# Kernel optimization log

Measured on AMD Instinct MI355X. Metric: run time of the kernel, lower is better.

The kernel has to match this reference:

```python
import jax
import jax.numpy as jnp
import numpy as np
from functools import partial

B, C_CLS, H, W = 1, 2, 480, 854
KS = (7, 7, 9)       # kernel sizes of the 3 pairwise kernels
DILS = (64, 16, 1)   # their dilations
STEPS = 5            # PacCRFLoose: independent params per mean-field step


def unfold2d(x, k, dil):
    """x: [B,C,H,W] -> [B,C,k*k,H,W]: zero-padded dilated k x k neighborhoods."""
    b, c, h, w = x.shape
    pad = (k // 2) * dil
    xp = jnp.pad(x, ((0, 0), (0, 0), (pad, pad), (pad, pad)))
    taps = [xp[:, :, i * dil:i * dil + h, j * dil:j * dil + w]
            for i in range(k) for j in range(k)]
    return jnp.stack(taps, axis=2)


@partial(jax.checkpoint, static_argnums=(1, 2))
def pac_kernel(feat, k, dil):
    """Fixed Gaussian pixel-adaptive kernel exp(-0.5*||f_p - f_q||^2): [B,k*k,H,W]."""
    d = unfold2d(feat, k, dil) - feat[:, :, None]  # center tap diff is 0 -> kernel 1
    return jnp.exp(-0.5 * jnp.sum(d * d, axis=1))


def message(Q, K, k, dil, filt):
    """PacConv2d with shared spatial filter: sum_t w_t * K_t(p) * Q(p + off_t)."""
    Qc = unfold2d(Q, k, dil)  # [B, C, T, H, W]
    return jnp.einsum('bcthw,bthw,t->bchw', Qc, K, filt)


def crf_forward(unary, x, feat_scales, potts_w, unary_weights, pw_weights,
                w_filt0, w_filt1, w_filt2, compat0, compat1):
    b, _, h, w = x.shape
    yy, xx = jnp.meshgrid(jnp.arange(h, dtype=x.dtype),
                          jnp.arange(w, dtype=x.dtype), indexing='ij')
    mesh = jnp.broadcast_to(jnp.stack([yy, xx])[None], (b, 2, h, w))

    # create_YXRGB: channels [y/s0, x/s1, r/s2, g/s3, b/s4]
    feats = [jnp.concatenate([mesh / feat_scales[i, :2, None, None],
                              x / feat_scales[i, 2:, None, None]], axis=1)
             for i in range(3)]
    # create_position_feats appended as 4th edge feature; PacCRF only consumes
    # edge_feat[0..n_kernels-1] so it is dead in the original forward too.
    _pos = mesh * (1.0 / potts_w.reshape(-1, 1, 1))

    # edge kernels are computed once (PacCRFLoose shares them across steps)
    kernels = [pac_kernel(feats[i], KS[i], DILS[i]) for i in range(3)]

    unary5 = unary * 5.0  # ModelWithCrf scales unary by 5 before the CRF

    def step(logQ, p):
        uw, pw, w0, w1, w2, c0, c1 = p
        Q = jax.nn.softmax(logQ, axis=1)
        m0 = jnp.einsum('dc,bchw->bdhw', c0, message(Q, kernels[0], KS[0], DILS[0], w0))
        m1 = jnp.einsum('dc,bchw->bdhw', c1, message(Q, kernels[1], KS[1], DILS[1], w1))
        m2 = message(Q, kernels[2], KS[2], DILS[2], w2)  # potts: no compat conv
        new_logQ = uw * unary5 + pw[0] * m0 + pw[1] * m1 + pw[2] * m2
        return new_logQ, None

    logQ, _ = jax.lax.scan(jax.checkpoint(step), unary5,
                           (unary_weights, pw_weights, w_filt0, w_filt1, w_filt2,
                            compat0, compat1))
    return logQ  # final_output='log_Q'


def setup_inputs():
    key = jax.random.key(0)
    k = jax.random.split(key, 8)
    unary = jax.random.normal(k[0], (B, C_CLS, H, W), jnp.float32)
    x = jax.random.uniform(k[1], (B, 3, H, W), jnp.float32) * 255.0  # RGB frame
    # p_sc = ((5-1)*16+1)/4 = 16.25, c_sc = 30.0 for all 3 scale sets (as in source)
    feat_scales = jnp.tile(jnp.array([16.25, 16.25, 30.0, 30.0, 30.0],
                                     jnp.float32)[None], (3, 1))
    potts_w = jnp.ones((1,), jnp.float32)
    unary_weights = jnp.full((STEPS,), 0.85, jnp.float32)
    pw_weights = jnp.tile(jnp.array([1.0, 1.0, 6.0], jnp.float32)[None], (STEPS, 1))
    pr = 0.001  # perturbed_init range
    w_filt0 = 1.0 / 49 + (jax.random.uniform(k[2], (STEPS, 49)) - 0.5) * pr
    w_filt1 = 1.0 / 49 + (jax.random.uniform(k[3], (STEPS, 49)) - 0.5) * pr
    w_filt2 = 1.0 / 81 + (jax.random.uniform(k[4], (STEPS, 81)) - 0.5) * pr
    off_diag = (1.0 - jnp.eye(C_CLS, dtype=jnp.float32))[None]
    compat0 = off_diag + (jax.random.uniform(k[5], (STEPS, C_CLS, C_CLS)) - 0.5) * pr
    compat1 = off_diag + (jax.random.uniform(k[6], (STEPS, C_CLS, C_CLS)) - 0.5) * pr
    return dict(unary=unary, x=x, feat_scales=feat_scales, potts_w=potts_w,
                unary_weights=unary_weights, pw_weights=pw_weights,
                w_filt0=w_filt0, w_filt1=w_filt1, w_filt2=w_filt2,
                compat0=compat0, compat1=compat1)


def reference(unary, x, feat_scales, potts_w, unary_weights, pw_weights,
              w_filt0, w_filt1, w_filt2, compat0, compat1):
    return crf_forward(unary, x, feat_scales, potts_w, unary_weights, pw_weights,
                       w_filt0, w_filt1, w_filt2, compat0, compat1)
```

## Files before the change

kernel.cpp:

```cpp
#include <hip/hip_runtime.h>

typedef _Float16 h2 __attribute__((ext_vector_type(2)));

#define HH 480
#define WW 854
#define HWSZ (HH * WW)
#define PAD 192
#define PSTR 1240
#define PH (HH + 2 * PAD)
#define PCELLS (PH * PSTR)
#define TPSTRIDE 240

#if __has_builtin(__builtin_amdgcn_exp2f)
#define EXP2(x) __builtin_amdgcn_exp2f(x)
#else
#define EXP2(x) exp2f(x)
#endif

__device__ __forceinline__ float fdot2f(h2 a, h2 b, float c)
{
#if __has_builtin(__builtin_amdgcn_fdot2)
    return __builtin_amdgcn_fdot2(a, b, c, false);
#else
    return fmaf((float)a.x, (float)b.x, fmaf((float)a.y, (float)b.y, c));
#endif
}

__device__ __forceinline__ h2 bch2(unsigned u)
{
    union { unsigned u; h2 h; } v; v.u = u; return v.h;
}
__device__ __forceinline__ unsigned h2u(h2 h)
{
    union { h2 h; unsigned u; } v; v.h = h; return v.u;
}
__device__ __forceinline__ float hiq(unsigned u)
{
    union { unsigned u; h2 h; } v; v.u = u; return (float)v.h.y;
}
__device__ __forceinline__ unsigned short hbits(_Float16 h)
{
    union { _Float16 h; unsigned short u; } v; v.h = h; return v.u;
}

__global__ __launch_bounds__(256) void init_P(
    const float* __restrict__ xrgb, const float* __restrict__ fs,
    uint2* __restrict__ PA, uint2* __restrict__ PB)
{
    int i = blockIdx.x * 256 + threadIdx.x;
    if (i >= PCELLS) return;
    int y = i / PSTR, x = i - y * PSTR;
    int iy = y - PAD, ix = x - PAD;
    uint2 v;
    if (iy >= 0 && iy < HH && ix >= 0 && ix < WW) {
        int p = iy * WW + ix;
        _Float16 rh = (_Float16)(xrgb[p] * (1.0f / fs[2]));
        _Float16 gh = (_Float16)(xrgb[HWSZ + p] * (1.0f / fs[3]));
        _Float16 bh = (_Float16)(xrgb[2 * HWSZ + p] * (1.0f / fs[4]));
        v = make_uint2(h2u(h2{rh, gh}), h2u(h2{bh, (_Float16)0}));
    } else {
        v = make_uint2(0x7BFF7BFFu, 0x00007BFFu);
    }
    PA[i] = v;
    PB[i] = v;
}

__global__ __launch_bounds__(256) void pack0(
    const float* __restrict__ unary, unsigned* __restrict__ PAw)
{
    int i = blockIdx.x * 256 + threadIdx.x;
    if (i >= HWSZ) return;
    float l0 = unary[i], l1 = unary[HWSZ + i];
    float q = 1.0f / (1.0f + __expf(5.0f * (l1 - l0)));
    int y = i / WW, x = i - y * WW;
    int c = (y + PAD) * PSTR + x + PAD;
    unsigned old = PAw[2 * c + 1];
    PAw[2 * c + 1] = (old & 0xFFFFu) | ((unsigned)hbits((_Float16)q) << 16);
}

__global__ __launch_bounds__(256) void build_tp(
    const float* __restrict__ fs, const float* __restrict__ uwArr,
    const float* __restrict__ pwArr,
    const float* __restrict__ w0, const float* __restrict__ w1,
    const float* __restrict__ w2,
    const float* __restrict__ c0, const float* __restrict__ c1,
    float* __restrict__ tp)
{
    int s = blockIdx.x;
    int t = threadIdx.x;
    float* d = tp + s * TPSTRIDE;
    const float NH = -0.72134752044448169f;

    if (t < 49) {
        int dy = t / 7 - 3, dx = t % 7 - 3;
        float py = dy * 64.0f / fs[0], px = dx * 64.0f / fs[1];
        d[(t / 7) * 8 + t % 7] =
            log2f(w0[s * 49 + t]) + NH * (py * py + px * px);
    } else if (t >= 64 && t < 113) {
        int u = t - 64;
        int dy = u / 7 - 3, dx = u % 7 - 3;
        float py = dy * 16.0f / fs[5], px = dx * 16.0f / fs[6];
        d[56 + (u / 7) * 8 + u % 7] =
            log2f(w1[s * 49 + u]) + NH * (py * py + px * px);
    } else if (t >= 128 && t < 209) {
        int u = t - 128;
        int dy = u / 9 - 4, dx = u % 9 - 4;
        float py = dy / fs[10], px = dx / fs[11];
        d[112 + (u / 9) * 12 + u % 9] =
            log2f(w2[s * 81 + u]) + NH * (py * py + px * px);
    } else if (t == 224) {
        float r1 = fs[2] / fs[7], r2 = fs[2] / fs[12];
        d[220] = NH;
        d[221] = NH * r1 * r1;
        d[222] = NH * r2 * r2;
        d[223] = c0[s * 4 + 0];  d[224] = c0[s * 4 + 1];
        d[225] = c0[s * 4 + 2];  d[226] = c0[s * 4 + 3];
        d[227] = c1[s * 4 + 0];  d[228] = c1[s * 4 + 1];
        d[229] = c1[s * 4 + 2];  d[230] = c1[s * 4 + 3];
        d[231] = pwArr[s * 3 + 0];
        d[232] = pwArr[s * 3 + 1];
        d[233] = pwArr[s * 3 + 2];
        d[234] = uwArr[s] * 5.0f;
    }
}

__device__ __forceinline__ void tap8(uint2 aq, h2 rgp, h2 bqp, float nk,
                                     float tpv, float& A, float& B)
{
    h2 drg = bch2(aq.x) - rgp;
    h2 dbq = bch2(aq.y) - bqp;
    h2 dbm = bch2(h2u(dbq) & 0xFFFFu);
    float s1 = fdot2f(drg, drg, 0.0f);
    float ssq = fdot2f(dbm, dbm, s1);
    float e = EXP2(fmaf(ssq, nk, tpv));
    A = fmaf(e, hiq(aq.y), A);
    B += e;
}

template <int T0, int N>
__device__ __forceinline__ void loadK0(uint2 (&buf)[N], const uint2* __restrict__ Pc)
{
#pragma unroll
    for (int t = 0; t < N; ++t) {
        const int tt = T0 + t;
        buf[t] = Pc[(tt / 7 - 3) * 64 * PSTR + (tt % 7 - 3) * 64];
    }
}
template <int T0, int N>
__device__ __forceinline__ void compK0(const uint2 (&buf)[N],
                                       const float* __restrict__ tp0,
                                       h2 rgp, h2 bqp, float nk,
                                       float& A, float& B)
{
#pragma unroll
    for (int t = 0; t < N; ++t) {
        const int tt = T0 + t;
        tap8(buf[t], rgp, bqp, nk, tp0[(tt / 7) * 8 + tt % 7], A, B);
    }
}
template <int T0, int N>
__device__ __forceinline__ void compK2(const uint2* __restrict__ T2b,
                                       const float* __restrict__ tp2,
                                       h2 rgp, h2 bqp, float nk,
                                       float& A, float& B)
{
#pragma unroll
    for (int t = 0; t < N; ++t) {
        const int tt = T0 + t;
        tap8(T2b[(tt / 9) * 136 + tt % 9], rgp, bqp, nk,
             tp2[(tt / 9) * 12 + tt % 9], A, B);
    }
}

template <bool LAST>
__global__ __launch_bounds__(256, 3) void crf_step(
    const uint2* __restrict__ srcP, unsigned* __restrict__ dstPw,
    const float* __restrict__ unary, const float* __restrict__ tpAll,
    int step, float* __restrict__ out)
{
    __shared__ uint2 T1[14 * 224];
    __shared__ uint2 T2[10 * 136];

    int tid = threadIdx.y * 128 + threadIdx.x;
    int x0 = blockIdx.x * 128, y0 = blockIdx.y * 2;

#pragma unroll
    for (int r = 0; r < 14; ++r) {
        if (tid < 112) {
            int gy = y0 + 16 * (r >> 1) + (r & 1) - 48;
            const uint4* srow = (const uint4*)
                (srcP + (gy + PAD) * PSTR + (x0 - 48 + PAD));
            ((uint4*)T1)[r * 112 + tid] = srow[tid];
        }
    }
#pragma unroll
    for (int r = 0; r < 10; ++r) {
        int t2 = tid - 128;
        if (t2 >= 0 && t2 < 68) {
            int gy = y0 - 4 + r;
            const uint4* srow = (const uint4*)
                (srcP + (gy + PAD) * PSTR + (x0 - 4 + PAD));
            ((uint4*)T2)[r * 68 + t2] = srow[t2];
        }
    }
    __syncthreads();

    int x = x0 + threadIdx.x;
    int y = y0 + threadIdx.y;
    if (x >= WW) return;
    int p = y * WW + x;
    int ccell = (y + PAD) * PSTR + x + PAD;

    const float* tp0 = tpAll + step * TPSTRIDE;
    const float* tp1 = tp0 + 56;
    const float* tp2 = tp0 + 112;
    const float* sc  = tp0 + 220;
    float nk0 = sc[0], nk1 = sc[1], nk2 = sc[2];

    float un0 = unary[p], un1 = unary[HWSZ + p];

    const uint2* Pc = srcP + ccell;
    uint2 cw = *Pc;
    h2 rgp = bch2(cw.x);
    h2 bqp = bch2(cw.y);

    const uint2* T1b = T1 + threadIdx.y * 224 + threadIdx.x;
    const uint2* T2b = T2 + threadIdx.y * 136 + threadIdx.x;

    float A0 = 0.f, B0 = 0.f, A1 = 0.f, B1 = 0.f, A2 = 0.f, B2 = 0.f;

    uint2 bA[13], bB[12], bC[12], bD[12];
    loadK0<0, 13>(bA, Pc);
    compK2<0, 20>(T2b, tp2, rgp, bqp, nk2, A2, B2);
    loadK0<13, 12>(bB, Pc);
    compK0<0, 13>(bA, tp0, rgp, bqp, nk0, A0, B0);
    compK2<20, 20>(T2b, tp2, rgp, bqp, nk2, A2, B2);
    loadK0<25, 12>(bC, Pc);
    compK0<13, 12>(bB, tp0, rgp, bqp, nk0, A0, B0);
    compK2<40, 20>(T2b, tp2, rgp, bqp, nk2, A2, B2);
    loadK0<37, 12>(bD, Pc);
    compK0<25, 12>(bC, tp0, rgp, bqp, nk0, A0, B0);
    compK2<60, 21>(T2b, tp2, rgp, bqp, nk2, A2, B2);
    compK0<37, 12>(bD, tp0, rgp, bqp, nk0, A0, B0);

#pragma unroll
    for (int i = 0; i < 7; ++i)
#pragma unroll
        for (int j = 0; j < 7; ++j)
            tap8(T1b[i * 448 + j * 16], rgp, bqp, nk1,
                 tp1[i * 8 + j], A1, B1);

    float m00 = A0, m01 = B0 - A0;
    float m10 = A1, m11 = B1 - A1;
    float m20 = A2, m21 = B2 - A2;

    float r00 = sc[3] * m00 + sc[4] * m01;
    float r01 = sc[5] * m00 + sc[6] * m01;
    float r10 = sc[7] * m10 + sc[8] * m11;
    float r11 = sc[9] * m10 + sc[10] * m11;

    float pw0 = sc[11], pw1 = sc[12], pw2 = sc[13], uw5 = sc[14];
    float o0 = uw5 * un0 + pw0 * r00 + pw1 * r10 + pw2 * m20;
    float o1 = uw5 * un1 + pw0 * r01 + pw1 * r11 + pw2 * m21;

    if (LAST) {
        out[p] = o0;
        out[HWSZ + p] = o1;
    } else {
        float qn = 1.0f / (1.0f + __expf(o1 - o0));
        unsigned nb = (h2u(bqp) & 0xFFFFu) |
                      ((unsigned)hbits((_Float16)qn) << 16);
        dstPw[2 * ccell + 1] = nb;
    }
}

extern "C" void kernel_launch(void* const* d_in, const int* in_sizes, int n_in,
                              void* d_out, int out_size, void* d_ws, size_t ws_size,
                              hipStream_t stream)
{
    const float* unary = (const float*)d_in[0];
    const float* xrgb  = (const float*)d_in[1];
    const float* fs    = (const float*)d_in[2];
    const float* uw    = (const float*)d_in[4];
    const float* pw    = (const float*)d_in[5];
    const float* w0    = (const float*)d_in[6];
    const float* w1    = (const float*)d_in[7];
    const float* w2    = (const float*)d_in[8];
    const float* c0    = (const float*)d_in[9];
    const float* c1    = (const float*)d_in[10];
    float* out = (float*)d_out;

    uint2* PA = (uint2*)d_ws;
    uint2* PB = (uint2*)((char*)d_ws + (size_t)PCELLS * 8);
    float* tpAll = (float*)((char*)d_ws + (size_t)PCELLS * 16);

    init_P<<<(PCELLS + 255) / 256, 256, 0, stream>>>(xrgb, fs, PA, PB);
    pack0<<<(HWSZ + 255) / 256, 256, 0, stream>>>(unary, (unsigned*)PA);
    build_tp<<<5, 256, 0, stream>>>(fs, uw, pw, w0, w1, w2, c0, c1, tpAll);

    dim3 gs((WW + 127) / 128, HH / 2), bs(128, 2);
    for (int s = 0; s < 5; ++s) {
        const uint2* src = (s & 1) ? PB : PA;
        unsigned* dst = (unsigned*)((s & 1) ? PA : PB);
        if (s < 4)
            crf_step<false><<<gs, bs, 0, stream>>>(src, dst, unary, tpAll,
                                                   s, out);
        else
            crf_step<true><<<gs, bs, 0, stream>>>(src, dst, unary, tpAll,
                                                  s, out);
    }
}
```

Before: 185.0 us.

## Issue dilated-tap global loads before barrier and interleave K1 taps

```diff
diff --git a/kernel.cpp b/kernel.cpp
--- a/kernel.cpp
+++ b/kernel.cpp
@@ -33,10 +33,6 @@
 __device__ __forceinline__ unsigned h2u(h2 h)
 {
     union { h2 h; unsigned u; } v; v.h = h; return v.u;
-}
-__device__ __forceinline__ float hiq(unsigned u)
-{
-    union { unsigned u; h2 h; } v; v.u = u; return (float)v.h.y;
 }
 __device__ __forceinline__ unsigned short hbits(_Float16 h)
 {
@@ -129,11 +125,11 @@
 {
     h2 drg = bch2(aq.x) - rgp;
     h2 dbq = bch2(aq.y) - bqp;
-    h2 dbm = bch2(h2u(dbq) & 0xFFFFu);
     float s1 = fdot2f(drg, drg, 0.0f);
-    float ssq = fdot2f(dbm, dbm, s1);
+    float db = (float)dbq.x;
+    float ssq = fmaf(db, db, s1);
     float e = EXP2(fmaf(ssq, nk, tpv));
-    A = fmaf(e, hiq(aq.y), A);
+    A = fmaf(e, (float)bch2(aq.y).y, A);
     B += e;
 }
 
@@ -159,6 +155,19 @@
     }
 }
 template <int T0, int N>
+__device__ __forceinline__ void compK1(const uint2* __restrict__ T1b,
+                                       const float* __restrict__ tp1,
+                                       h2 rgp, h2 bqp, float nk,
+                                       float& A, float& B)
+{
+#pragma unroll
+    for (int t = 0; t < N; ++t) {
+        const int tt = T0 + t;
+        tap8(T1b[(tt / 7) * 448 + (tt % 7) * 16], rgp, bqp, nk,
+             tp1[(tt / 7) * 8 + tt % 7], A, B);
+    }
+}
+template <int T0, int N>
 __device__ __forceinline__ void compK2(const uint2* __restrict__ T2b,
                                        const float* __restrict__ tp2,
                                        h2 rgp, h2 bqp, float nk,
@@ -173,7 +182,7 @@
 }
 
 template <bool LAST>
-__global__ __launch_bounds__(256, 3) void crf_step(
+__global__ __launch_bounds__(256, 4) void crf_step(
     const uint2* __restrict__ srcP, unsigned* __restrict__ dstPw,
     const float* __restrict__ unary, const float* __restrict__ tpAll,
     int step, float* __restrict__ out)
@@ -203,11 +212,9 @@
             ((uint4*)T2)[r * 68 + t2] = srow[t2];
         }
     }
-    __syncthreads();
 
     int x = x0 + threadIdx.x;
     int y = y0 + threadIdx.y;
-    if (x >= WW) return;
     int p = y * WW + x;
     int ccell = (y + PAD) * PSTR + x + PAD;
 
@@ -217,10 +224,19 @@
     const float* sc  = tp0 + 220;
     float nk0 = sc[0], nk1 = sc[1], nk2 = sc[2];
 
-    float un0 = unary[p], un1 = unary[HWSZ + p];
-
     const uint2* Pc = srcP + ccell;
-    uint2 cw = *Pc;
+    uint2 cw = make_uint2(0u, 0u);
+    float un0 = 0.f, un1 = 0.f;
+    uint2 bA[13];
+    bool act = (x < WW);
+    if (act) {
+        cw = *Pc;
+        un0 = unary[p]; un1 = unary[HWSZ + p];
+        loadK0<0, 13>(bA, Pc);
+    }
+    __syncthreads();
+    if (!act) return;
+
     h2 rgp = bch2(cw.x);
     h2 bqp = bch2(cw.y);
 
@@ -229,26 +245,20 @@
 
     float A0 = 0.f, B0 = 0.f, A1 = 0.f, B1 = 0.f, A2 = 0.f, B2 = 0.f;
 
-    uint2 bA[13], bB[12], bC[12], bD[12];
-    loadK0<0, 13>(bA, Pc);
+    uint2 bB[12], bC[12], bD[12];
+    loadK0<13, 12>(bB, Pc);
     compK2<0, 20>(T2b, tp2, rgp, bqp, nk2, A2, B2);
-    loadK0<13, 12>(bB, Pc);
     compK0<0, 13>(bA, tp0, rgp, bqp, nk0, A0, B0);
+    loadK0<25, 12>(bC, Pc);
     compK2<20, 20>(T2b, tp2, rgp, bqp, nk2, A2, B2);
-    loadK0<25, 12>(bC, Pc);
     compK0<13, 12>(bB, tp0, rgp, bqp, nk0, A0, B0);
+    loadK0<37, 12>(bD, Pc);
+    compK1<0, 25>(T1b, tp1, rgp, bqp, nk1, A1, B1);
+    compK0<25, 12>(bC, tp0, rgp, bqp, nk0, A0, B0);
     compK2<40, 20>(T2b, tp2, rgp, bqp, nk2, A2, B2);
-    loadK0<37, 12>(bD, Pc);
-    compK0<25, 12>(bC, tp0, rgp, bqp, nk0, A0, B0);
+    compK0<37, 12>(bD, tp0, rgp, bqp, nk0, A0, B0);
+    compK1<25, 24>(T1b, tp1, rgp, bqp, nk1, A1, B1);
     compK2<60, 21>(T2b, tp2, rgp, bqp, nk2, A2, B2);
-    compK0<37, 12>(bD, tp0, rgp, bqp, nk0, A0, B0);
-
-#pragma unroll
-    for (int i = 0; i < 7; ++i)
-#pragma unroll
-        for (int j = 0; j < 7; ++j)
-            tap8(T1b[i * 448 + j * 16], rgp, bqp, nk1,
-                 tp1[i * 8 + j], A1, B1);
 
     float m00 = A0, m01 = B0 - A0;
     float m10 = A1, m11 = B1 - A1;
```

Result: faster. 167.8 us (-9.3%).

## Process two horizontal pixels per thread with 128-bit loads and 4-row tiles

Applied to the files above, without the earlier changes.

```diff
diff --git a/kernel.cpp b/kernel.cpp
--- a/kernel.cpp
+++ b/kernel.cpp
@@ -33,10 +33,6 @@
 __device__ __forceinline__ unsigned h2u(h2 h)
 {
     union { h2 h; unsigned u; } v; v.h = h; return v.u;
-}
-__device__ __forceinline__ float hiq(unsigned u)
-{
-    union { unsigned u; h2 h; } v; v.u = u; return (float)v.h.y;
 }
 __device__ __forceinline__ unsigned short hbits(_Float16 h)
 {
@@ -129,87 +125,105 @@
 {
     h2 drg = bch2(aq.x) - rgp;
     h2 dbq = bch2(aq.y) - bqp;
-    h2 dbm = bch2(h2u(dbq) & 0xFFFFu);
     float s1 = fdot2f(drg, drg, 0.0f);
-    float ssq = fdot2f(dbm, dbm, s1);
+    float db = (float)dbq.x;
+    float ssq = fmaf(db, db, s1);
     float e = EXP2(fmaf(ssq, nk, tpv));
-    A = fmaf(e, hiq(aq.y), A);
+    A = fmaf(e, (float)bch2(aq.y).y, A);
     B += e;
 }
 
-template <int T0, int N>
-__device__ __forceinline__ void loadK0(uint2 (&buf)[N], const uint2* __restrict__ Pc)
+__device__ __forceinline__ void tapPair(uint4 a, h2 rg0, h2 bq0, h2 rg1, h2 bq1,
+                                        float nk, float tpv,
+                                        float& Aa, float& Ba, float& Ab, float& Bb)
+{
+    tap8(make_uint2(a.x, a.y), rg0, bq0, nk, tpv, Aa, Ba);
+    tap8(make_uint2(a.z, a.w), rg1, bq1, nk, tpv, Ab, Bb);
+}
+
+template <int I>
+__device__ __forceinline__ void loadRow64(uint4 (&buf)[7], const uint2* __restrict__ Pc)
 {
 #pragma unroll
-    for (int t = 0; t < N; ++t) {
-        const int tt = T0 + t;
-        buf[t] = Pc[(tt / 7 - 3) * 64 * PSTR + (tt % 7 - 3) * 64];
-    }
-}
-template <int T0, int N>
-__device__ __forceinline__ void compK0(const uint2 (&buf)[N],
-                                       const float* __restrict__ tp0,
-                                       h2 rgp, h2 bqp, float nk,
-                                       float& A, float& B)
+    for (int j = 0; j < 7; ++j)
+        buf[j] = *(const uint4*)(Pc + (I - 3) * 64 * PSTR + (j - 3) * 64);
+}
+template <int I>
+__device__ __forceinline__ void compRow64(const uint4 (&buf)[7],
+    const float* __restrict__ tp0, h2 rg0, h2 bq0, h2 rg1, h2 bq1, float nk,
+    float& Aa, float& Ba, float& Ab, float& Bb)
 {
 #pragma unroll
-    for (int t = 0; t < N; ++t) {
-        const int tt = T0 + t;
-        tap8(buf[t], rgp, bqp, nk, tp0[(tt / 7) * 8 + tt % 7], A, B);
-    }
-}
-template <int T0, int N>
-__device__ __forceinline__ void compK2(const uint2* __restrict__ T2b,
-                                       const float* __restrict__ tp2,
-                                       h2 rgp, h2 bqp, float nk,
-                                       float& A, float& B)
+    for (int j = 0; j < 7; ++j)
+        tapPair(buf[j], rg0, bq0, rg1, bq1, nk, tp0[I * 8 + j], Aa, Ba, Ab, Bb);
+}
+
+template <int I>
+__device__ __forceinline__ void compK1row(const uint4* __restrict__ T1l,
+    const float* __restrict__ tp1, h2 rg0, h2 bq0, h2 rg1, h2 bq1, float nk,
+    float& Aa, float& Ba, float& Ab, float& Bb)
 {
 #pragma unroll
-    for (int t = 0; t < N; ++t) {
-        const int tt = T0 + t;
-        tap8(T2b[(tt / 9) * 136 + tt % 9], rgp, bqp, nk,
-             tp2[(tt / 9) * 12 + tt % 9], A, B);
+    for (int j = 0; j < 7; ++j) {
+        uint4 a = T1l[I * 448 + 8 * j];
+        tapPair(a, rg0, bq0, rg1, bq1, nk, tp1[I * 8 + j], Aa, Ba, Ab, Bb);
+    }
+}
+
+template <int I>
+__device__ __forceinline__ void compK2row(const uint4* __restrict__ T2r,
+    const uint2* __restrict__ T2r2,
+    const float* __restrict__ tp2, h2 rg0, h2 bq0, h2 rg1, h2 bq1, float nk,
+    float& Aa, float& Ba, float& Ab, float& Bb)
+{
+#pragma unroll
+    for (int j = 0; j < 9; ++j) {
+        float tpv = tp2[I * 12 + j];
+        if ((j & 1) == 0) {
+            uint4 a = T2r[I * 68 + j / 2];
+            tapPair(a, rg0, bq0, rg1, bq1, nk, tpv, Aa, Ba, Ab, Bb);
+        } else {
+            uint2 c0 = T2r2[I * 136 + j];
+            uint2 c1 = T2r2[I * 136 + j + 1];
+            tap8(c0, rg0, bq0, nk, tpv, Aa, Ba);
+            tap8(c1, rg1, bq1, nk, tpv, Ab, Bb);
+        }
     }
 }
 
 template <bool LAST>
-__global__ __launch_bounds__(256, 3) void crf_step(
+__global__ __launch_bounds__(256, 2) void crf_step(
     const uint2* __restrict__ srcP, unsigned* __restrict__ dstPw,
     const float* __restrict__ unary, const float* __restrict__ tpAll,
     int step, float* __restrict__ out)
 {
-    __shared__ uint2 T1[14 * 224];
-    __shared__ uint2 T2[10 * 136];
-
-    int tid = threadIdx.y * 128 + threadIdx.x;
-    int x0 = blockIdx.x * 128, y0 = blockIdx.y * 2;
-
-#pragma unroll
-    for (int r = 0; r < 14; ++r) {
-        if (tid < 112) {
-            int gy = y0 + 16 * (r >> 1) + (r & 1) - 48;
-            const uint4* srow = (const uint4*)
-                (srcP + (gy + PAD) * PSTR + (x0 - 48 + PAD));
-            ((uint4*)T1)[r * 112 + tid] = srow[tid];
-        }
-    }
-#pragma unroll
-    for (int r = 0; r < 10; ++r) {
-        int t2 = tid - 128;
-        if (t2 >= 0 && t2 < 68) {
-            int gy = y0 - 4 + r;
-            const uint4* srow = (const uint4*)
-                (srcP + (gy + PAD) * PSTR + (x0 - 4 + PAD));
-            ((uint4*)T2)[r * 68 + t2] = srow[t2];
-        }
-    }
-    __syncthreads();
-
-    int x = x0 + threadIdx.x;
-    int y = y0 + threadIdx.y;
-    if (x >= WW) return;
-    int p = y * WW + x;
-    int ccell = (y + PAD) * PSTR + x + PAD;
+    __shared__ uint4 T1[28 * 112];
+    __shared__ uint4 T2[12 * 68];
+
+    int tx = threadIdx.x, ty = threadIdx.y;
+    int tid = ty * 64 + tx;
+    int x0 = blockIdx.x * 128, y0 = blockIdx.y * 4;
+
+    for (int c = tid; c < 28 * 112; c += 256) {
+        int r = c / 112, col = c - r * 112;
+        int gy = y0 + (r & 3) + 16 * ((r >> 2) - 3);
+        T1[c] = *(const uint4*)
+            (srcP + (gy + PAD) * PSTR + (x0 - 48 + PAD) + 2 * col);
+    }
+    for (int c = tid; c < 12 * 68; c += 256) {
+        int r = c / 68, col = c - r * 68;
+        int gy = y0 - 4 + r;
+        T2[c] = *(const uint4*)
+            (srcP + (gy + PAD) * PSTR + (x0 - 4 + PAD) + 2 * col);
+    }
+
+    int px = x0 + 2 * tx;
+    int y = y0 + ty;
+    bool act = (px < WW);
+    int p = y * WW + px;
+    int pSafe = act ? p : 0;
+    int ccell = (y + PAD) * PSTR + px + PAD;
+    const uint2* Pc = srcP + ccell;
 
     const float* tp0 = tpAll + step * TPSTRIDE;
     const float* tp1 = tp0 + 56;
@@ -217,60 +231,87 @@
     const float* sc  = tp0 + 220;
     float nk0 = sc[0], nk1 = sc[1], nk2 = sc[2];
 
-    float un0 = unary[p], un1 = unary[HWSZ + p];
-
-    const uint2* Pc = srcP + ccell;
-    uint2 cw = *Pc;
-    h2 rgp = bch2(cw.x);
-    h2 bqp = bch2(cw.y);
-
-    const uint2* T1b = T1 + threadIdx.y * 224 + threadIdx.x;
-    const uint2* T2b = T2 + threadIdx.y * 136 + threadIdx.x;
-
-    float A0 = 0.f, B0 = 0.f, A1 = 0.f, B1 = 0.f, A2 = 0.f, B2 = 0.f;
-
-    uint2 bA[13], bB[12], bC[12], bD[12];
-    loadK0<0, 13>(bA, Pc);
-    compK2<0, 20>(T2b, tp2, rgp, bqp, nk2, A2, B2);
-    loadK0<13, 12>(bB, Pc);
-    compK0<0, 13>(bA, tp0, rgp, bqp, nk0, A0, B0);
-    compK2<20, 20>(T2b, tp2, rgp, bqp, nk2, A2, B2);
-    loadK0<25, 12>(bC, Pc);
-    compK0<13, 12>(bB, tp0, rgp, bqp, nk0, A0, B0);
-    compK2<40, 20>(T2b, tp2, rgp, bqp, nk2, A2, B2);
-    loadK0<37, 12>(bD, Pc);
-    compK0<25, 12>(bC, tp0, rgp, bqp, nk0, A0, B0);
-    compK2<60, 21>(T2b, tp2, rgp, bqp, nk2, A2, B2);
-    compK0<37, 12>(bD, tp0, rgp, bqp, nk0, A0, B0);
-
-#pragma unroll
-    for (int i = 0; i < 7; ++i)
-#pragma unroll
-        for (int j = 0; j < 7; ++j)
-            tap8(T1b[i * 448 + j * 16], rgp, bqp, nk1,
-                 tp1[i * 8 + j], A1, B1);
-
-    float m00 = A0, m01 = B0 - A0;
-    float m10 = A1, m11 = B1 - A1;
-    float m20 = A2, m21 = B2 - A2;
-
-    float r00 = sc[3] * m00 + sc[4] * m01;
-    float r01 = sc[5] * m00 + sc[6] * m01;
-    float r10 = sc[7] * m10 + sc[8] * m11;
-    float r11 = sc[9] * m10 + sc[10] * m11;
+    uint4 cw = *(const uint4*)Pc;
+    float2 unc0 = *(const float2*)(unary + pSafe);
+    float2 unc1 = *(const float2*)(unary + HWSZ + pSafe);
+    uint4 bufA[7], bufB[7];
+    loadRow64<0>(bufA, Pc);
+    loadRow64<1>(bufB, Pc);
+    __syncthreads();
+
+    h2 rg0 = bch2(cw.x), bq0 = bch2(cw.y);
+    h2 rg1 = bch2(cw.z), bq1 = bch2(cw.w);
+
+    const uint4* T1l  = T1 + ty * 112 + tx;
+    const uint4* T2r  = T2 + ty * 68 + tx;
+    const uint2* T2r2 = (const uint2*)T2 + ty * 136 + 2 * tx;
+
+    float A0a = 0, B0a = 0, A0b = 0, B0b = 0;
+    float A1a = 0, B1a = 0, A1b = 0, B1b = 0;
+    float A2a = 0, B2a = 0, A2b = 0, B2b = 0;
+
+#define K2(I) compK2row<I>(T2r, T2r2, tp2, rg0, bq0, rg1, bq1, nk2, A2a, B2a, A2b, B2b)
+#define K1(I) compK1row<I>(T1l, tp1, rg0, bq0, rg1, bq1, nk1, A1a, B1a, A1b, B1b)
+#define K0C(B_, I) compRow64<I>(B_, tp0, rg0, bq0, rg1, bq1, nk0, A0a, B0a, A0b, B0b)
+
+    K2(0);
+    K0C(bufA, 0);  loadRow64<2>(bufA, Pc);
+    K2(1);
+    K1(0);
+    K0C(bufB, 1);  loadRow64<3>(bufB, Pc);
+    K2(2);
+    K1(1);
+    K0C(bufA, 2);  loadRow64<4>(bufA, Pc);
+    K2(3);
+    K1(2);
+    K0C(bufB, 3);  loadRow64<5>(bufB, Pc);
+    K2(4);
+    K1(3);
+    K0C(bufA, 4);  loadRow64<6>(bufA, Pc);
+    K2(5);
+    K1(4);
+    K0C(bufB, 5);
+    K2(6);
+    K1(5);
+    K0C(bufA, 6);
+    K2(7);
+    K1(6);
+    K2(8);
+
+#undef K2
+#undef K1
+#undef K0C
+
+    if (!act) return;
 
     float pw0 = sc[11], pw1 = sc[12], pw2 = sc[13], uw5 = sc[14];
-    float o0 = uw5 * un0 + pw0 * r00 + pw1 * r10 + pw2 * m20;
-    float o1 = uw5 * un1 + pw0 * r01 + pw1 * r11 + pw2 * m21;
+
+    float m01a = B0a - A0a, m11a = B1a - A1a, m21a = B2a - A2a;
+    float r00a = sc[3] * A0a + sc[4] * m01a;
+    float r01a = sc[5] * A0a + sc[6] * m01a;
+    float r10a = sc[7] * A1a + sc[8] * m11a;
+    float r11a = sc[9] * A1a + sc[10] * m11a;
+    float o0a = uw5 * unc0.x + pw0 * r00a + pw1 * r10a + pw2 * A2a;
+    float o1a = uw5 * unc1.x + pw0 * r01a + pw1 * r11a + pw2 * m21a;
+
+    float m01b = B0b - A0b, m11b = B1b - A1b, m21b = B2b - A2b;
+    float r00b = sc[3] * A0b + sc[4] * m01b;
+    float r01b = sc[5] * A0b + sc[6] * m01b;
+    float r10b = sc[7] * A1b + sc[8] * m11b;
+    float r11b = sc[9] * A1b + sc[10] * m11b;
+    float o0b = uw5 * unc0.y + pw0 * r00b + pw1 * r10b + pw2 * A2b;
+    float o1b = uw5 * unc1.y + pw0 * r01b + pw1 * r11b + pw2 * m21b;
 
     if (LAST) {
-        out[p] = o0;
-        out[HWSZ + p] = o1;
+        *(float2*)(out + p) = make_float2(o0a, o0b);
+        *(float2*)(out + HWSZ + p) = make_float2(o1a, o1b);
     } else {
-        float qn = 1.0f / (1.0f + __expf(o1 - o0));
-        unsigned nb = (h2u(bqp) & 0xFFFFu) |
-                      ((unsigned)hbits((_Float16)qn) << 16);
-        dstPw[2 * ccell + 1] = nb;
+        float qa = 1.0f / (1.0f + __expf(o1a - o0a));
+        float qb = 1.0f / (1.0f + __expf(o1b - o0b));
+        dstPw[2 * ccell + 1] = (cw.y & 0xFFFFu) |
+                               ((unsigned)hbits((_Float16)qa) << 16);
+        dstPw[2 * ccell + 3] = (cw.w & 0xFFFFu) |
+                               ((unsigned)hbits((_Float16)qb) << 16);
     }
 }
 
@@ -298,7 +339,7 @@
     pack0<<<(HWSZ + 255) / 256, 256, 0, stream>>>(unary, (unsigned*)PA);
     build_tp<<<5, 256, 0, stream>>>(fs, uw, pw, w0, w1, w2, c0, c1, tpAll);
 
-    dim3 gs((WW + 127) / 128, HH / 2), bs(128, 2);
+    dim3 gs((WW + 127) / 128, HH / 4), bs(64, 4);
     for (int s = 0; s < 5; ++s) {
         const uint2* src = (s & 1) ? PB : PA;
         unsigned* dst = (unsigned*)((s & 1) ? PA : PB);
```

Measured after the change: 229.2 us. 23.9% more time.
